# Kernel tuning notes

Hardware: AMD Instinct MI355X
Metric: run time of the kernel (lower is better)

## Reference

```python
import jax, jax.numpy as jnp
import numpy as np
import math

N_QUBITS = 8
N_QLAYERS = 1
LN_EPS = 1e-5


def _rx(state, theta, wire, n):
    # state: (N, 2,...,2) complex64 with n qubit axes; theta: (N,)
    sh = (theta.shape[0],) + (1,) * (n - 1)
    c = jnp.cos(theta / 2).reshape(sh)
    s = jnp.sin(theta / 2).reshape(sh)
    a = jax.lax.index_in_dim(state, 0, wire + 1, keepdims=False)
    b = jax.lax.index_in_dim(state, 1, wire + 1, keepdims=False)
    return jnp.stack([c * a - 1j * s * b, -1j * s * a + c * b], axis=wire + 1)


def _cnot(state, cw, tw, n):
    s0 = jax.lax.index_in_dim(state, 0, cw + 1, keepdims=False)
    s1 = jax.lax.index_in_dim(state, 1, cw + 1, keepdims=False)
    t_ax = tw + 1 if tw < cw else tw  # target axis index after removing control axis
    s1 = jnp.flip(s1, axis=t_ax)
    return jnp.stack([s0, s1], axis=cw + 1)


def _quantum(angles, qweights):
    # AngleEmbedding (RX) + BasicEntanglerLayers (RX + CNOT ring) + PauliZ expvals
    # angles: (N, 8) float; qweights: (1, 8) float -> returns (N, 8) float
    n = N_QUBITS
    N = angles.shape[0]
    state = jnp.zeros((N,) + (2,) * n, jnp.complex64)
    state = state.at[(slice(None),) + (0,) * n].set(1.0 + 0j)
    for w in range(n):
        state = _rx(state, angles[:, w], w, n)
    for l in range(N_QLAYERS):
        for w in range(n):
            state = _rx(state, jnp.broadcast_to(qweights[l, w], (N,)), w, n)
        for cw in range(n):
            state = _cnot(state, cw, (cw + 1) % n, n)
    probs = state.real ** 2 + state.imag ** 2
    zs = []
    for w in range(n):
        p = probs.sum(axis=tuple(a for a in range(1, n + 1) if a != w + 1))  # (N, 2)
        zs.append(p[:, 0] - p[:, 1])
    return jnp.stack(zs, axis=-1)


def _layernorm(x, g, b):
    m = x.mean(-1, keepdims=True)
    v = ((x - m) ** 2).mean(-1, keepdims=True)
    return (x - m) / jnp.sqrt(v + LN_EPS) * g + b


def _forward(x, Wq, Wk, Wv, Wo, ln1_g, ln1_b, W1, b1, W2, b2, ln2_g, ln2_b,
             ql1_w, ql1_b, qweights, ql2_w, ql2_b):
    B, S, D = x.shape
    H = 16
    dk = D // H
    q = (x @ Wq.T).reshape(B, S, H, dk)
    k = (x @ Wk.T).reshape(B, S, H, dk)
    v = (x @ Wv.T).reshape(B, S, H, dk)
    scores = jnp.einsum('bqhd,bkhd->bhqk', q, k) * (1.0 / math.sqrt(dk))
    attn = jax.nn.softmax(scores, axis=-1)
    o = jnp.einsum('bhqk,bkhd->bqhd', attn, v).reshape(B, S, D) @ Wo.T
    x = _layernorm(o + x, ln1_g, ln1_b)
    ff = jax.nn.relu(x @ W1.T + b1) @ W2.T + b2
    x = _layernorm(ff + x, ln2_g, ln2_b)
    angles = (x @ ql1_w.T + ql1_b).reshape(B * S, N_QUBITS)
    z = _quantum(angles, qweights).reshape(B, S, N_QUBITS).astype(x.dtype)
    y = jnp.concatenate([z, x], axis=2) @ ql2_w.T + ql2_b
    return y


def setup_inputs() -> dict:
    key = jax.random.key(0)
    ks = jax.random.split(key, 12)
    B, S, D, F = 4, 1024, 1024, 4096
    sc = 0.02
    w = lambda k, *sh: jax.random.normal(k, sh, jnp.float32) * sc
    return {
        'x': jax.random.normal(ks[0], (B, S, D), jnp.float32),
        'Wq': w(ks[1], D, D), 'Wk': w(ks[2], D, D), 'Wv': w(ks[3], D, D), 'Wo': w(ks[4], D, D),
        'ln1_g': jnp.ones((D,), jnp.float32), 'ln1_b': jnp.zeros((D,), jnp.float32),
        'W1': w(ks[5], F, D), 'b1': jnp.zeros((F,), jnp.float32),
        'W2': w(ks[6], D, F), 'b2': jnp.zeros((D,), jnp.float32),
        'ln2_g': jnp.ones((D,), jnp.float32), 'ln2_b': jnp.zeros((D,), jnp.float32),
        'ql1_w': w(ks[7], N_QUBITS, D), 'ql1_b': jnp.zeros((N_QUBITS,), jnp.float32),
        'qweights': jax.random.uniform(ks[8], (N_QLAYERS, N_QUBITS), jnp.float32, 0.0, 2 * np.pi),
        'ql2_w': w(ks[9], D, D + N_QUBITS), 'ql2_b': jnp.zeros((D,), jnp.float32),
    }


def reference(x, Wq, Wk, Wv, Wo, ln1_g, ln1_b, W1, b1, W2, b2, ln2_g, ln2_b,
              ql1_w, ql1_b, qweights, ql2_w, ql2_b):
    return _forward(x, Wq, Wk, Wv, Wo, ln1_g, ln1_b, W1, b1, W2, b2, ln2_g, ln2_b,
                    ql1_w, ql1_b, qweights, ql2_w, ql2_b)
```

## Files before the change

kernel.cpp:

```cpp
#include <hip/hip_runtime.h>
#include <hip/hip_bf16.h>

typedef __bf16 bf16_t;
typedef __attribute__((ext_vector_type(8))) __bf16 bf16x8;
typedef __attribute__((ext_vector_type(4))) float floatx4;

#define BM 128
#define BK 32

enum { EPI_NONE = 0, EPI_RESID, EPI_BIAS_RELU, EPI_BIAS_RESID, EPI_QL2 };

__device__ __forceinline__ void gld_lds16(const bf16_t* g, bf16_t* l) {
  __builtin_amdgcn_global_load_lds(
      (__attribute__((address_space(1))) void*)(g),
      (__attribute__((address_space(3))) void*)(l), 16, 0, 0);
}

__device__ __forceinline__ void core128(const bf16_t* __restrict__ Ag,
                                        const bf16_t* __restrict__ Bg,
                                        int K, int ldb,
                                        bf16_t* As, bf16_t* Bs,
                                        floatx4 acc[4][4]) {
  const int tid = threadIdx.x;
  const int wid = tid >> 6, lane = tid & 63;
  const int wm = (wid >> 1) * 64, wn = (wid & 1) * 64;
  const int m16 = lane & 15, quad = lane >> 4;
  for (int k0 = 0; k0 < K; k0 += BK) {
    #pragma unroll
    for (int i = 0; i < 2; ++i) {
      int ci = i * 256 + tid;
      int row = ci >> 2, cc = ci & 3;
      gld_lds16(Ag + (size_t)row * K + k0 + cc * 8, As + ci * 8);
      gld_lds16(Bg + (size_t)row * ldb + k0 + cc * 8, Bs + ci * 8);
    }
    __syncthreads();
    bf16x8 af[4], bfr[4];
    #pragma unroll
    for (int mt = 0; mt < 4; ++mt)
      af[mt] = *(const bf16x8*)&As[(wm + mt * 16 + m16) * BK + quad * 8];
    #pragma unroll
    for (int nt = 0; nt < 4; ++nt)
      bfr[nt] = *(const bf16x8*)&Bs[(wn + nt * 16 + m16) * BK + quad * 8];
    #pragma unroll
    for (int mt = 0; mt < 4; ++mt)
      #pragma unroll
      for (int nt = 0; nt < 4; ++nt)
        acc[mt][nt] = __builtin_amdgcn_mfma_f32_16x16x32_bf16(af[mt], bfr[nt], acc[mt][nt], 0, 0, 0);
    __syncthreads();
  }
}

template<int EPI>
__global__ __launch_bounds__(256)
void gemm128(const bf16_t* __restrict__ A, const bf16_t* __restrict__ B,
             bf16_t* __restrict__ C, const float* __restrict__ bias,
             int N, int K) {
  __shared__ bf16_t As[BM * BK];
  __shared__ bf16_t Bs[BM * BK];
  const int tid = threadIdx.x;
  const int wid = tid >> 6, lane = tid & 63;
  const int wm = (wid >> 1) * 64, wn = (wid & 1) * 64;
  const int m16 = lane & 15, quad = lane >> 4;
  const int m0 = blockIdx.y * BM, n0 = blockIdx.x * BM;
  floatx4 acc[4][4];
  const floatx4 vzero = {0.f, 0.f, 0.f, 0.f};
  #pragma unroll
  for (int mt = 0; mt < 4; ++mt)
    #pragma unroll
    for (int nt = 0; nt < 4; ++nt) acc[mt][nt] = vzero;
  core128(A + (size_t)m0 * K, B + (size_t)n0 * K, K, K, As, Bs, acc);
  #pragma unroll
  for (int mt = 0; mt < 4; ++mt)
    #pragma unroll
    for (int nt = 0; nt < 4; ++nt) {
      const int gcol = n0 + wn + nt * 16 + m16;
      float bv = (EPI == EPI_BIAS_RELU) ? bias[gcol] : 0.f;
      #pragma unroll
      for (int r = 0; r < 4; ++r) {
        const int grow = m0 + wm + mt * 16 + quad * 4 + r;
        float v = acc[mt][nt][r];
        if (EPI == EPI_BIAS_RELU) { v += bv; v = fmaxf(v, 0.f); }
        C[(size_t)grow * N + gcol] = (bf16_t)v;
      }
    }
}

__global__ __launch_bounds__(256)
void gemm_qkv(const bf16_t* __restrict__ X, const bf16_t* __restrict__ Wb,
              bf16_t* __restrict__ Qo, bf16_t* __restrict__ Ko, bf16_t* __restrict__ Vt) {
  __shared__ bf16_t As[BM * BK];
  __shared__ bf16_t Bs[BM * BK];
  const int tid = threadIdx.x;
  const int wid = tid >> 6, lane = tid & 63;
  const int wm = (wid >> 1) * 64, wn = (wid & 1) * 64;
  const int m16 = lane & 15, quad = lane >> 4;
  const int m0 = blockIdx.y * BM, n0 = blockIdx.x * BM;
  const int sel = blockIdx.z;
  const bf16_t* B = Wb + (size_t)sel * 1024 * 1024;
  floatx4 acc[4][4];
  const floatx4 vzero = {0.f, 0.f, 0.f, 0.f};
  #pragma unroll
  for (int mt = 0; mt < 4; ++mt)
    #pragma unroll
    for (int nt = 0; nt < 4; ++nt) acc[mt][nt] = vzero;
  core128(X + (size_t)m0 * 1024, B + (size_t)n0 * 1024, 1024, 1024, As, Bs, acc);
  if (sel < 2) {
    bf16_t* C = sel ? Ko : Qo;
    const float sc = sel ? 1.f : 0.125f;
    #pragma unroll
    for (int mt = 0; mt < 4; ++mt)
      #pragma unroll
      for (int nt = 0; nt < 4; ++nt) {
        const int gcol = n0 + wn + nt * 16 + m16;
        #pragma unroll
        for (int r = 0; r < 4; ++r) {
          const int grow = m0 + wm + mt * 16 + quad * 4 + r;
          C[(size_t)grow * 1024 + gcol] = (bf16_t)(acc[mt][nt][r] * sc);
        }
      }
  } else {
    #pragma unroll
    for (int mt = 0; mt < 4; ++mt) {
      const int grow0 = m0 + wm + mt * 16 + quad * 4;
      const int b = grow0 >> 10, s = grow0 & 1023;
      #pragma unroll
      for (int nt = 0; nt < 4; ++nt) {
        const int gcol = n0 + wn + nt * 16 + m16;
        const int h = gcol >> 6, d = gcol & 63;
        #pragma unroll
        for (int r = 0; r < 4; ++r)
          Vt[(((size_t)b * 16 + h) * 64 + d) * 1024 + s + r] = (bf16_t)acc[mt][nt][r];
      }
    }
  }
}

template<int EPI, bool OUTF32>
__global__ __launch_bounds__(256)
void gemm64(const bf16_t* __restrict__ A, const bf16_t* __restrict__ B,
            void* __restrict__ Cv,
            const bf16_t* __restrict__ resid, const float* __restrict__ bias,
            const bf16_t* __restrict__ z, const float* __restrict__ zw,
            int N, int K, int ldb, int boff) {
  __shared__ bf16_t As[2][BM * 32];
  __shared__ bf16_t Bs[2][64 * 32];
  const int tid = threadIdx.x;
  const int wid = tid >> 6, lane = tid & 63;
  const int wm = (wid >> 1) * 64, wn = (wid & 1) * 32;
  const int m16 = lane & 15, quad = lane >> 4;
  const int m0 = blockIdx.y * BM, n0 = blockIdx.x * 64;
  const bf16_t* Ag = A + (size_t)m0 * K;
  const bf16_t* Bg = B + (size_t)n0 * ldb + boff;
  floatx4 acc[4][2];
  const floatx4 vzero = {0.f, 0.f, 0.f, 0.f};
  #pragma unroll
  for (int mt = 0; mt < 4; ++mt)
    #pragma unroll
    for (int nt = 0; nt < 2; ++nt) acc[mt][nt] = vzero;
  const int brow = tid >> 2;
  for (int k0 = 0; k0 < K; k0 += 64) {
    #pragma unroll
    for (int ks = 0; ks < 2; ++ks) {
      #pragma unroll
      for (int i = 0; i < 2; ++i) {
        int ci = i * 256 + tid;
        int row = ci >> 2, cc = ci & 3;
        gld_lds16(Ag + (size_t)row * K + k0 + ks * 32 + cc * 8, &As[ks][ci * 8]);
      }
      gld_lds16(Bg + (size_t)brow * ldb + k0 + ks * 32 + (tid & 3) * 8, &Bs[ks][tid * 8]);
    }
    __syncthreads();
    #pragma unroll
    for (int ks = 0; ks < 2; ++ks) {
      bf16x8 af[4], bfr[2];
      #pragma unroll
      for (int mt = 0; mt < 4; ++mt)
        af[mt] = *(const bf16x8*)&As[ks][(wm + mt * 16 + m16) * 32 + quad * 8];
      #pragma unroll
      for (int nt = 0; nt < 2; ++nt)
        bfr[nt] = *(const bf16x8*)&Bs[ks][(wn + nt * 16 + m16) * 32 + quad * 8];
      #pragma unroll
      for (int mt = 0; mt < 4; ++mt)
        #pragma unroll
        for (int nt = 0; nt < 2; ++nt)
          acc[mt][nt] = __builtin_amdgcn_mfma_f32_16x16x32_bf16(af[mt], bfr[nt], acc[mt][nt], 0, 0, 0);
    }
    __syncthreads();
  }
  #pragma unroll
  for (int mt = 0; mt < 4; ++mt)
    #pragma unroll
    for (int nt = 0; nt < 2; ++nt) {
      const int gcol = n0 + wn + nt * 16 + m16;
      float bv = 0.f;
      if (EPI == EPI_BIAS_RESID || EPI == EPI_QL2) bv = bias[gcol];
      #pragma unroll
      for (int r = 0; r < 4; ++r) {
        const int grow = m0 + wm + mt * 16 + quad * 4 + r;
        float v = acc[mt][nt][r];
        if (EPI == EPI_RESID) v += (float)resid[(size_t)grow * N + gcol];
        if (EPI == EPI_BIAS_RESID) v += bv + (float)resid[(size_t)grow * N + gcol];
        if (EPI == EPI_QL2) {
          float s = 0.f;
          #pragma unroll
          for (int u = 0; u < 8; ++u)
            s += (float)z[(size_t)grow * 8 + u] * zw[(size_t)gcol * 1032 + u];
          v += bv + s;
        }
        if (OUTF32) ((float*)Cv)[(size_t)grow * N + gcol] = v;
        else        ((bf16_t*)Cv)[(size_t)grow * N + gcol] = (bf16_t)v;
      }
    }
}

__global__ __launch_bounds__(256)
void attn_kernel(const bf16_t* __restrict__ Q, const bf16_t* __restrict__ Kb,
                 const bf16_t* __restrict__ Vt, bf16_t* __restrict__ O) {
  __shared__ bf16_t Qs[64 * 64];
  __shared__ bf16_t Ks[128 * 64];
  __shared__ bf16_t Vs[64 * 128];
  __shared__ bf16_t Ps[4][16 * 128];
  const int tid = threadIdx.x;
  const int wid = tid >> 6, lane = tid & 63;
  const int m16 = lane & 15, quad = lane >> 4;
  const int qt = blockIdx.x, bh = blockIdx.y;
  const int b = bh >> 4, h = bh & 15;
  const size_t qbase = ((size_t)(b * 1024 + qt * 64)) * 1024 + h * 64;
  #pragma unroll
  for (int i = 0; i < 2; ++i) {
    int ci = i * 256 + tid;
    int row = ci >> 3, cc = ci & 7;
    *(bf16x8*)&Qs[row * 64 + ((cc ^ (row & 7)) * 8)] =
        *(const bf16x8*)&Q[qbase + (size_t)row * 1024 + cc * 8];
  }
  __syncthreads();
  const int qm = wid * 16 + m16;
  bf16x8 qf0 = *(const bf16x8*)&Qs[qm * 64 + ((quad ^ (qm & 7)) * 8)];
  bf16x8 qf1 = *(const bf16x8*)&Qs[qm * 64 + (((4 + quad) ^ (qm & 7)) * 8)];
  floatx4 oacc[4];
  float rs[4];
  const floatx4 vzero = {0.f, 0.f, 0.f, 0.f};
  #pragma unroll
  for (int dt = 0; dt < 4; ++dt) oacc[dt] = vzero;
  #pragma unroll
  for (int r = 0; r < 4; ++r) rs[r] = 0.f;
  const size_t kbase = ((size_t)(b * 1024)) * 1024 + h * 64;
  const size_t vbase = ((size_t)bh * 64) * 1024;
  for (int kt = 0; kt < 8; ++kt) {
    __syncthreads();
    #pragma unroll
    for (int i = 0; i < 4; ++i) {
      int ci = i * 256 + tid;
      int row = ci >> 3, cc = ci & 7;
      *(bf16x8*)&Ks[row * 64 + ((cc ^ (row & 7)) * 8)] =
          *(const bf16x8*)&Kb[kbase + (size_t)(kt * 128 + row) * 1024 + cc * 8];
    }
    #pragma unroll
    for (int i = 0; i < 4; ++i) {
      int ci = i * 256 + tid;
      int dr = ci >> 4, cc = ci & 15;
      int gs = (cc & 8) | ((cc & 7) ^ (dr & 7));
      *(bf16x8*)&Vs[dr * 128 + gs * 8] =
          *(const bf16x8*)&Vt[vbase + (size_t)dr * 1024 + kt * 128 + cc * 8];
    }
    __syncthreads();
    floatx4 sa[8];
    #pragma unroll
    for (int nt = 0; nt < 8; ++nt) sa[nt] = vzero;
    #pragma unroll
    for (int nt = 0; nt < 8; ++nt) {
      const int n = nt * 16 + m16;
      bf16x8 kf0 = *(const bf16x8*)&Ks[n * 64 + ((quad ^ (n & 7)) * 8)];
      bf16x8 kf1 = *(const bf16x8*)&Ks[n * 64 + (((4 + quad) ^ (n & 7)) * 8)];
      sa[nt] = __builtin_amdgcn_mfma_f32_16x16x32_bf16(qf0, kf0, sa[nt], 0, 0, 0);
      sa[nt] = __builtin_amdgcn_mfma_f32_16x16x32_bf16(qf1, kf1, sa[nt], 0, 0, 0);
    }
    #pragma unroll
    for (int nt = 0; nt < 8; ++nt)
      #pragma unroll
      for (int r = 0; r < 4; ++r) {
        float pv = __expf(sa[nt][r]);
        rs[r] += pv;
        const int prow = quad * 4 + r;
        const int g = nt * 2 + (m16 >> 3);
        const int gs = (g & 8) | ((g & 7) ^ (prow & 7));
        Ps[wid][prow * 128 + gs * 8 + (m16 & 7)] = (bf16_t)pv;
      }
    bf16x8 pf[4];
    #pragma unroll
    for (int ksub = 0; ksub < 4; ++ksub) {
      const int g = ksub * 4 + quad;
      const int gs = (g & 8) | ((g & 7) ^ (m16 & 7));
      pf[ksub] = *(const bf16x8*)&Ps[wid][m16 * 128 + gs * 8];
    }
    #pragma unroll
    for (int dt = 0; dt < 4; ++dt) {
      const int n = dt * 16 + m16;
      #pragma unroll
      for (int ksub = 0; ksub < 4; ++ksub) {
        const int g = ksub * 4 + quad;
        const int gs = (g & 8) | ((g & 7) ^ (n & 7));
        bf16x8 vf = *(const bf16x8*)&Vs[n * 128 + gs * 8];
        oacc[dt] = __builtin_amdgcn_mfma_f32_16x16x32_bf16(pf[ksub], vf, oacc[dt], 0, 0, 0);
      }
    }
  }
  #pragma unroll
  for (int r = 0; r < 4; ++r) {
    rs[r] += __shfl_xor(rs[r], 1);
    rs[r] += __shfl_xor(rs[r], 2);
    rs[r] += __shfl_xor(rs[r], 4);
    rs[r] += __shfl_xor(rs[r], 8);
  }
  const size_t obase = ((size_t)(b * 1024 + qt * 64 + wid * 16)) * 1024 + h * 64;
  #pragma unroll
  for (int dt = 0; dt < 4; ++dt)
    #pragma unroll
    for (int r = 0; r < 4; ++r)
      O[obase + (size_t)(quad * 4 + r) * 1024 + dt * 16 + m16] = (bf16_t)(oacc[dt][r] / rs[r]);
}

__global__ __launch_bounds__(256)
void conv_kernel(const float* __restrict__ in, bf16_t* __restrict__ out, int n8) {
  for (int i = blockIdx.x * 256 + threadIdx.x; i < n8; i += gridDim.x * 256) {
    const float* p = in + (size_t)i * 8;
    floatx4 a = *(const floatx4*)p;
    floatx4 b = *(const floatx4*)(p + 4);
    bf16x8 o;
    #pragma unroll
    for (int j = 0; j < 4; ++j) { o[j] = (bf16_t)a[j]; o[4 + j] = (bf16_t)b[j]; }
    *(bf16x8*)(out + (size_t)i * 8) = o;
  }
}

__global__ __launch_bounds__(256)
void ln_kernel(const bf16_t* __restrict__ in, const float* __restrict__ g,
               const float* __restrict__ b, bf16_t* __restrict__ out) {
  const int row = blockIdx.x * 4 + (threadIdx.x >> 6);
  const int lane = threadIdx.x & 63;
  const bf16_t* p = in + (size_t)row * 1024 + lane * 16;
  bf16x8 v0 = *(const bf16x8*)p;
  bf16x8 v1 = *(const bf16x8*)(p + 8);
  float f[16];
  #pragma unroll
  for (int j = 0; j < 8; ++j) { f[j] = (float)v0[j]; f[8 + j] = (float)v1[j]; }
  float s = 0.f, ss = 0.f;
  #pragma unroll
  for (int j = 0; j < 16; ++j) { s += f[j]; ss += f[j] * f[j]; }
  #pragma unroll
  for (int off = 1; off < 64; off <<= 1) { s += __shfl_xor(s, off); ss += __shfl_xor(ss, off); }
  const float m = s * (1.f / 1024.f);
  const float inv_sd = rsqrtf(ss * (1.f / 1024.f) - m * m + 1e-5f);
  const float* gp = g + lane * 16;
  const float* bp = b + lane * 16;
  bf16x8 o0, o1;
  #pragma unroll
  for (int j = 0; j < 8; ++j) o0[j] = (bf16_t)((f[j] - m) * inv_sd * gp[j] + bp[j]);
  #pragma unroll
  for (int j = 0; j < 8; ++j) o1[j] = (bf16_t)((f[8 + j] - m) * inv_sd * gp[8 + j] + bp[8 + j]);
  *(bf16x8*)&out[(size_t)row * 1024 + lane * 16] = o0;
  *(bf16x8*)&out[(size_t)row * 1024 + lane * 16 + 8] = o1;
}

__global__ __launch_bounds__(256)
void quantum_kernel(const bf16_t* __restrict__ x2, const float* __restrict__ qw1,
                    const float* __restrict__ qb1, const float* __restrict__ qwt,
                    bf16_t* __restrict__ z) {
  const int row = blockIdx.x * 4 + (threadIdx.x >> 6);
  const int lane = threadIdx.x & 63;
  const bf16_t* xp = x2 + (size_t)row * 1024 + lane * 16;
  bf16x8 xv0 = *(const bf16x8*)xp;
  bf16x8 xv1 = *(const bf16x8*)(xp + 8);
  float th[8];
  #pragma unroll
  for (int qq = 0; qq < 8; ++qq) {
    const float* wp = qw1 + (size_t)qq * 1024 + lane * 16;
    float s = 0.f;
    #pragma unroll
    for (int j = 0; j < 8; ++j) s += (float)xv0[j] * wp[j] + (float)xv1[j] * wp[8 + j];
    #pragma unroll
    for (int off = 1; off < 64; off <<= 1) s += __shfl_xor(s, off);
    th[qq] = s + qb1[qq] + qwt[qq];
  }
  if (lane == 0) {
    float c[8];
    #pragma unroll
    for (int qq = 0; qq < 8; ++qq) c[qq] = cosf(th[qq]);
    float z0 = 1.f;
    #pragma unroll
    for (int u = 1; u < 8; ++u) z0 *= c[u];
    z[(size_t)row * 8 + 0] = (bf16_t)z0;
    float p = c[0];
    #pragma unroll
    for (int w = 1; w < 8; ++w) { p *= c[w]; z[(size_t)row * 8 + w] = (bf16_t)p; }
  }
}

extern "C" void kernel_launch(void* const* d_in, const int* in_sizes, int n_in,
                              void* d_out, int out_size, void* d_ws, size_t ws_size,
                              hipStream_t stream) {
  const float* x    = (const float*)d_in[0];
  const float* Wq   = (const float*)d_in[1];
  const float* Wk   = (const float*)d_in[2];
  const float* Wv   = (const float*)d_in[3];
  const float* Wo   = (const float*)d_in[4];
  const float* ln1g = (const float*)d_in[5];
  const float* ln1b = (const float*)d_in[6];
  const float* W1   = (const float*)d_in[7];
  const float* b1   = (const float*)d_in[8];
  const float* W2   = (const float*)d_in[9];
  const float* b2   = (const float*)d_in[10];
  const float* ln2g = (const float*)d_in[11];
  const float* ln2b = (const float*)d_in[12];
  const float* qw1  = (const float*)d_in[13];
  const float* qb1  = (const float*)d_in[14];
  const float* qwt  = (const float*)d_in[15];
  const float* ql2w = (const float*)d_in[16];
  const float* ql2b = (const float*)d_in[17];
  bf16_t* ws = (bf16_t*)d_ws;

  const size_t T = (size_t)4096 * 1024;
  bf16_t* outlo = (bf16_t*)d_out;
  bf16_t* outhi = outlo + T;

  bf16_t* xb    = ws;
  bf16_t* kb    = ws + T;
  bf16_t* vt    = ws + 2 * T;
  bf16_t* ff    = ws + 3 * T;
  bf16_t* wqkvb = ff;
  bf16_t* wob   = ff;
  bf16_t* w1b   = vt;
  bf16_t* w2b   = kb;
  bf16_t* ql2wb = vt;
  bf16_t* q     = outlo;
  bf16_t* o     = outhi;
  bf16_t* x1p   = outlo;
  bf16_t* x1    = outhi;
  bf16_t* x2p   = outlo;
  bf16_t* x2    = xb;
  bf16_t* z     = kb;

  const int M1 = 1024 * 1024 / 8, M4 = 4096 * 1024 / 8;
  conv_kernel<<<2048, 256, 0, stream>>>(x, xb, M4);
  conv_kernel<<<512, 256, 0, stream>>>(Wq, wqkvb, M1);
  conv_kernel<<<512, 256, 0, stream>>>(Wk, wqkvb + T / 4, M1);
  conv_kernel<<<512, 256, 0, stream>>>(Wv, wqkvb + T / 2, M1);
  gemm_qkv<<<dim3(8, 32, 3), 256, 0, stream>>>(xb, wqkvb, q, kb, vt);
  attn_kernel<<<dim3(16, 64), 256, 0, stream>>>(q, kb, vt, o);
  conv_kernel<<<512, 256, 0, stream>>>(Wo, wob, M1);
  gemm64<EPI_RESID, false><<<dim3(16, 32), 256, 0, stream>>>(
      o, wob, x1p, xb, nullptr, nullptr, nullptr, 1024, 1024, 1024, 0);
  ln_kernel<<<1024, 256, 0, stream>>>(x1p, ln1g, ln1b, x1);
  conv_kernel<<<2048, 256, 0, stream>>>(W1, w1b, M4);
  gemm128<EPI_BIAS_RELU><<<dim3(32, 32), 256, 0, stream>>>(x1, w1b, ff, b1, 4096, 1024);
  conv_kernel<<<2048, 256, 0, stream>>>(W2, w2b, M4);
  gemm64<EPI_BIAS_RESID, false><<<dim3(16, 32), 256, 0, stream>>>(
      ff, w2b, x2p, x1, b2, nullptr, nullptr, 1024, 4096, 4096, 0);
  ln_kernel<<<1024, 256, 0, stream>>>(x2p, ln2g, ln2b, x2);
  quantum_kernel<<<1024, 256, 0, stream>>>(x2, qw1, qb1, qwt, z);
  conv_kernel<<<512, 256, 0, stream>>>(ql2w, ql2wb, 1024 * 1032 / 8);
  gemm64<EPI_QL2, true><<<dim3(16, 32), 256, 0, stream>>>(
      x2, ql2wb, d_out, nullptr, ql2b, z, ql2w, 1024, 1024, 1032, 8);
}
```

Before: 429.3 us.

## Deepen GEMM K-tiles with XOR-swizzled LDS staging and batch weight conversions

The GEMM cores now stage larger K slices per barrier: 64 in gemm128/qkv and 128 in gemm64. Global loads go directly to LDS using an XOR swizzle of 16-byte chunks, so the row-strided fragment reads avoid bank conflicts. This halves or quarters the number of sync rounds and reduces LDS conflicts, at the cost of more LDS per block, which may lower occupancy. Separately, the many fp32-to-bf16 conversion launches are merged into multi-segment launches. W1 and W2 are now converted together before the FFN, and Wo gets its own workspace slot so it can be converted up front.

```diff
diff --git a/kernel.cpp b/kernel.cpp
--- a/kernel.cpp
+++ b/kernel.cpp
@@ -6,7 +6,6 @@
 typedef __attribute__((ext_vector_type(4))) float floatx4;
 
 #define BM 128
-#define BK 32
 
 enum { EPI_NONE = 0, EPI_RESID, EPI_BIAS_RELU, EPI_BIAS_RESID, EPI_QL2 };
 
@@ -14,6 +13,18 @@
   __builtin_amdgcn_global_load_lds(
       (__attribute__((address_space(1))) void*)(g),
       (__attribute__((address_space(3))) void*)(l), 16, 0, 0);
+}
+
+template<int ROWS, int COLS>
+__device__ __forceinline__ void stage_swz(const bf16_t* g, int ld, bf16_t* lds, int tid) {
+  constexpr int G = COLS / 8;
+  #pragma unroll
+  for (int i = 0; i < ROWS * G / 256; ++i) {
+    int ci = i * 256 + tid;
+    int row = ci / G, cc = ci % G;
+    int gg = (G == 8) ? (cc ^ (row & 7)) : ((cc & 8) | ((cc & 7) ^ (row & 7)));
+    gld_lds16(g + (size_t)row * ld + gg * 8, lds + ci * 8);
+  }
 }
 
 __device__ __forceinline__ void core128(const bf16_t* __restrict__ Ag,
@@ -25,27 +36,28 @@
   const int wid = tid >> 6, lane = tid & 63;
   const int wm = (wid >> 1) * 64, wn = (wid & 1) * 64;
   const int m16 = lane & 15, quad = lane >> 4;
-  for (int k0 = 0; k0 < K; k0 += BK) {
-    #pragma unroll
-    for (int i = 0; i < 2; ++i) {
-      int ci = i * 256 + tid;
-      int row = ci >> 2, cc = ci & 3;
-      gld_lds16(Ag + (size_t)row * K + k0 + cc * 8, As + ci * 8);
-      gld_lds16(Bg + (size_t)row * ldb + k0 + cc * 8, Bs + ci * 8);
-    }
-    __syncthreads();
-    bf16x8 af[4], bfr[4];
-    #pragma unroll
-    for (int mt = 0; mt < 4; ++mt)
-      af[mt] = *(const bf16x8*)&As[(wm + mt * 16 + m16) * BK + quad * 8];
-    #pragma unroll
-    for (int nt = 0; nt < 4; ++nt)
-      bfr[nt] = *(const bf16x8*)&Bs[(wn + nt * 16 + m16) * BK + quad * 8];
-    #pragma unroll
-    for (int mt = 0; mt < 4; ++mt)
+  const int r7 = m16 & 7;
+  for (int k0 = 0; k0 < K; k0 += 64) {
+    stage_swz<128, 64>(Ag + k0, K, As, tid);
+    stage_swz<128, 64>(Bg + k0, ldb, Bs, tid);
+    __syncthreads();
+    #pragma unroll
+    for (int ks = 0; ks < 2; ++ks) {
+      const int gi = ks * 4 + quad;
+      const int slot = gi ^ r7;
+      bf16x8 af[4], bfr[4];
+      #pragma unroll
+      for (int mt = 0; mt < 4; ++mt)
+        af[mt] = *(const bf16x8*)&As[((wm + mt * 16 + m16) * 8 + slot) * 8];
       #pragma unroll
       for (int nt = 0; nt < 4; ++nt)
-        acc[mt][nt] = __builtin_amdgcn_mfma_f32_16x16x32_bf16(af[mt], bfr[nt], acc[mt][nt], 0, 0, 0);
+        bfr[nt] = *(const bf16x8*)&Bs[((wn + nt * 16 + m16) * 8 + slot) * 8];
+      #pragma unroll
+      for (int mt = 0; mt < 4; ++mt)
+        #pragma unroll
+        for (int nt = 0; nt < 4; ++nt)
+          acc[mt][nt] = __builtin_amdgcn_mfma_f32_16x16x32_bf16(af[mt], bfr[nt], acc[mt][nt], 0, 0, 0);
+    }
     __syncthreads();
   }
 }
@@ -55,8 +67,8 @@
 void gemm128(const bf16_t* __restrict__ A, const bf16_t* __restrict__ B,
              bf16_t* __restrict__ C, const float* __restrict__ bias,
              int N, int K) {
-  __shared__ bf16_t As[BM * BK];
-  __shared__ bf16_t Bs[BM * BK];
+  __shared__ bf16_t As[BM * 64];
+  __shared__ bf16_t Bs[BM * 64];
   const int tid = threadIdx.x;
   const int wid = tid >> 6, lane = tid & 63;
   const int wm = (wid >> 1) * 64, wn = (wid & 1) * 64;
@@ -88,8 +100,8 @@
 __global__ __launch_bounds__(256)
 void gemm_qkv(const bf16_t* __restrict__ X, const bf16_t* __restrict__ Wb,
               bf16_t* __restrict__ Qo, bf16_t* __restrict__ Ko, bf16_t* __restrict__ Vt) {
-  __shared__ bf16_t As[BM * BK];
-  __shared__ bf16_t Bs[BM * BK];
+  __shared__ bf16_t As[BM * 64];
+  __shared__ bf16_t Bs[BM * 64];
   const int tid = threadIdx.x;
   const int wid = tid >> 6, lane = tid & 63;
   const int wm = (wid >> 1) * 64, wn = (wid & 1) * 64;
@@ -142,12 +154,13 @@
             const bf16_t* __restrict__ resid, const float* __restrict__ bias,
             const bf16_t* __restrict__ z, const float* __restrict__ zw,
             int N, int K, int ldb, int boff) {
-  __shared__ bf16_t As[2][BM * 32];
-  __shared__ bf16_t Bs[2][64 * 32];
+  __shared__ bf16_t As[BM * 128];
+  __shared__ bf16_t Bs[64 * 128];
   const int tid = threadIdx.x;
   const int wid = tid >> 6, lane = tid & 63;
   const int wm = (wid >> 1) * 64, wn = (wid & 1) * 32;
   const int m16 = lane & 15, quad = lane >> 4;
+  const int r7 = m16 & 7;
   const int m0 = blockIdx.y * BM, n0 = blockIdx.x * 64;
   const bf16_t* Ag = A + (size_t)m0 * K;
   const bf16_t* Bg = B + (size_t)n0 * ldb + boff;
@@ -157,28 +170,21 @@
   for (int mt = 0; mt < 4; ++mt)
     #pragma unroll
     for (int nt = 0; nt < 2; ++nt) acc[mt][nt] = vzero;
-  const int brow = tid >> 2;
-  for (int k0 = 0; k0 < K; k0 += 64) {
-    #pragma unroll
-    for (int ks = 0; ks < 2; ++ks) {
-      #pragma unroll
-      for (int i = 0; i < 2; ++i) {
-        int ci = i * 256 + tid;
-        int row = ci >> 2, cc = ci & 3;
-        gld_lds16(Ag + (size_t)row * K + k0 + ks * 32 + cc * 8, &As[ks][ci * 8]);
-      }
-      gld_lds16(Bg + (size_t)brow * ldb + k0 + ks * 32 + (tid & 3) * 8, &Bs[ks][tid * 8]);
-    }
-    __syncthreads();
-    #pragma unroll
-    for (int ks = 0; ks < 2; ++ks) {
+  for (int k0 = 0; k0 < K; k0 += 128) {
+    stage_swz<128, 128>(Ag + k0, K, As, tid);
+    stage_swz<64, 128>(Bg + k0, ldb, Bs, tid);
+    __syncthreads();
+    #pragma unroll
+    for (int ks = 0; ks < 4; ++ks) {
+      const int gi = ks * 4 + quad;
+      const int slot = (gi & 8) | ((gi & 7) ^ r7);
       bf16x8 af[4], bfr[2];
       #pragma unroll
       for (int mt = 0; mt < 4; ++mt)
-        af[mt] = *(const bf16x8*)&As[ks][(wm + mt * 16 + m16) * 32 + quad * 8];
+        af[mt] = *(const bf16x8*)&As[((wm + mt * 16 + m16) * 16 + slot) * 8];
       #pragma unroll
       for (int nt = 0; nt < 2; ++nt)
-        bfr[nt] = *(const bf16x8*)&Bs[ks][(wn + nt * 16 + m16) * 32 + quad * 8];
+        bfr[nt] = *(const bf16x8*)&Bs[((wn + nt * 16 + m16) * 16 + slot) * 8];
       #pragma unroll
       for (int mt = 0; mt < 4; ++mt)
         #pragma unroll
@@ -320,8 +326,17 @@
       O[obase + (size_t)(quad * 4 + r) * 1024 + dt * 16 + m16] = (bf16_t)(oacc[dt][r] / rs[r]);
 }
 
-__global__ __launch_bounds__(256)
-void conv_kernel(const float* __restrict__ in, bf16_t* __restrict__ out, int n8) {
+struct Segs {
+  const float* s[5];
+  bf16_t* d[5];
+  int n8[5];
+};
+__global__ __launch_bounds__(256)
+void conv_multi(Segs sg) {
+  const int zz = blockIdx.z;
+  const float* in = sg.s[zz];
+  bf16_t* out = sg.d[zz];
+  const int n8 = sg.n8[zz];
   for (int i = blockIdx.x * 256 + threadIdx.x; i < n8; i += gridDim.x * 256) {
     const float* p = in + (size_t)i * 8;
     floatx4 a = *(const floatx4*)p;
@@ -420,6 +435,7 @@
   bf16_t* ws = (bf16_t*)d_ws;
 
   const size_t T = (size_t)4096 * 1024;
+  const size_t M1 = (size_t)1024 * 1024;
   bf16_t* outlo = (bf16_t*)d_out;
   bf16_t* outhi = outlo + T;
 
@@ -428,7 +444,7 @@
   bf16_t* vt    = ws + 2 * T;
   bf16_t* ff    = ws + 3 * T;
   bf16_t* wqkvb = ff;
-  bf16_t* wob   = ff;
+  bf16_t* wob   = ff + 3 * M1;
   bf16_t* w1b   = vt;
   bf16_t* w2b   = kb;
   bf16_t* ql2wb = vt;
@@ -440,25 +456,43 @@
   bf16_t* x2    = xb;
   bf16_t* z     = kb;
 
-  const int M1 = 1024 * 1024 / 8, M4 = 4096 * 1024 / 8;
-  conv_kernel<<<2048, 256, 0, stream>>>(x, xb, M4);
-  conv_kernel<<<512, 256, 0, stream>>>(Wq, wqkvb, M1);
-  conv_kernel<<<512, 256, 0, stream>>>(Wk, wqkvb + T / 4, M1);
-  conv_kernel<<<512, 256, 0, stream>>>(Wv, wqkvb + T / 2, M1);
+  {
+    Segs sg;
+    sg.s[0] = x;  sg.d[0] = xb;            sg.n8[0] = (int)(T / 8);
+    sg.s[1] = Wq; sg.d[1] = wqkvb;         sg.n8[1] = (int)(M1 / 8);
+    sg.s[2] = Wk; sg.d[2] = wqkvb + M1;    sg.n8[2] = (int)(M1 / 8);
+    sg.s[3] = Wv; sg.d[3] = wqkvb + 2*M1;  sg.n8[3] = (int)(M1 / 8);
+    sg.s[4] = Wo; sg.d[4] = wob;           sg.n8[4] = (int)(M1 / 8);
+    conv_multi<<<dim3(512, 1, 5), 256, 0, stream>>>(sg);
+  }
   gemm_qkv<<<dim3(8, 32, 3), 256, 0, stream>>>(xb, wqkvb, q, kb, vt);
   attn_kernel<<<dim3(16, 64), 256, 0, stream>>>(q, kb, vt, o);
-  conv_kernel<<<512, 256, 0, stream>>>(Wo, wob, M1);
   gemm64<EPI_RESID, false><<<dim3(16, 32), 256, 0, stream>>>(
       o, wob, x1p, xb, nullptr, nullptr, nullptr, 1024, 1024, 1024, 0);
   ln_kernel<<<1024, 256, 0, stream>>>(x1p, ln1g, ln1b, x1);
-  conv_kernel<<<2048, 256, 0, stream>>>(W1, w1b, M4);
+  {
+    Segs sg;
+    sg.s[0] = W1; sg.d[0] = w1b; sg.n8[0] = (int)(T / 8);
+    sg.s[1] = W2; sg.d[1] = w2b; sg.n8[1] = (int)(T / 8);
+    sg.s[2] = nullptr; sg.d[2] = nullptr; sg.n8[2] = 0;
+    sg.s[3] = nullptr; sg.d[3] = nullptr; sg.n8[3] = 0;
+    sg.s[4] = nullptr; sg.d[4] = nullptr; sg.n8[4] = 0;
+    conv_multi<<<dim3(1024, 1, 2), 256, 0, stream>>>(sg);
+  }
   gemm128<EPI_BIAS_RELU><<<dim3(32, 32), 256, 0, stream>>>(x1, w1b, ff, b1, 4096, 1024);
-  conv_kernel<<<2048, 256, 0, stream>>>(W2, w2b, M4);
   gemm64<EPI_BIAS_RESID, false><<<dim3(16, 32), 256, 0, stream>>>(
       ff, w2b, x2p, x1, b2, nullptr, nullptr, 1024, 4096, 4096, 0);
   ln_kernel<<<1024, 256, 0, stream>>>(x2p, ln2g, ln2b, x2);
   quantum_kernel<<<1024, 256, 0, stream>>>(x2, qw1, qb1, qwt, z);
-  conv_kernel<<<512, 256, 0, stream>>>(ql2w, ql2wb, 1024 * 1032 / 8);
+  {
+    Segs sg;
+    sg.s[0] = ql2w; sg.d[0] = ql2wb; sg.n8[0] = 1024 * 1032 / 8;
+    sg.s[1] = nullptr; sg.d[1] = nullptr; sg.n8[1] = 0;
+    sg.s[2] = nullptr; sg.d[2] = nullptr; sg.n8[2] = 0;
+    sg.s[3] = nullptr; sg.d[3] = nullptr; sg.n8[3] = 0;
+    sg.s[4] = nullptr; sg.d[4] = nullptr; sg.n8[4] = 0;
+    conv_multi<<<dim3(512, 1, 1), 256, 0, stream>>>(sg);
+  }
   gemm64<EPI_QL2, true><<<dim3(16, 32), 256, 0, stream>>>(
       x2, ql2wb, d_out, nullptr, ql2b, z, ql2w, 1024, 1024, 1032, 8);
 }
```

Result: faster. 409.1 us (-4.7%).
